# Kernel tuning notes

Measured on AMD Instinct MI355X. Metric: run time of the kernel, lower is better.

## Reference

```python
import jax, jax.numpy as jnp
import numpy as np

N = 2097152

def _net(x, W1, b1, W2, b2, W3, b3):
    # Net: 4 -> 64 -> 64 -> 1 MLP with ReLU
    h = jax.nn.relu(x @ W1 + b1)
    h = jax.nn.relu(h @ W2 + b2)
    return h @ W3 + b3  # [..., 1]

def setup_inputs() -> dict:
    key = jax.random.key(0)
    ks = jax.random.split(key, 7)
    def init_w(k, fan_in, fan_out):
        return (jax.random.normal(k, (fan_in, fan_out), jnp.float32)
                * np.float32(np.sqrt(2.0 / fan_in)))
    return {
        "states": jax.random.normal(ks[0], (N, 4), jnp.float32),
        "W1": init_w(ks[1], 4, 64),
        "b1": jnp.zeros((64,), jnp.float32),
        "W2": init_w(ks[2], 64, 64),
        "b2": jnp.zeros((64,), jnp.float32),
        "W3": init_w(ks[3], 64, 1),
        "b3": jnp.zeros((1,), jnp.float32),
    }

def reference(states, W1, b1, W2, b2, W3, b3):
    # log Q(s) = net(s) - log(sum_i exp(net(e_i))) ; loss = -sum_s log Q(s)
    logits = _net(states, W1, b1, W2, b2, W3, b3)            # [N, 1]
    denom_logits = _net(jnp.eye(4, dtype=states.dtype),       # 4 one-hot states
                        W1, b1, W2, b2, W3, b3)               # [4, 1]
    log_denom = jax.nn.logsumexp(denom_logits)                # scalar
    n = jnp.asarray(states.shape[0], states.dtype)
    loss = -(jnp.sum(logits) - n * log_denom)
    return loss.reshape(1)  # original accumulates shape-[1] tensors
```

## Files before the change

kernel.cpp:

```cpp
#include <hip/hip_runtime.h>
#include <hip/hip_bf16.h>
#include <hip/hip_fp16.h>
#include <stdint.h>

typedef __bf16 bf16x8 __attribute__((ext_vector_type(8)));
typedef float  f32x4  __attribute__((ext_vector_type(4)));
typedef _Float16 h2   __attribute__((ext_vector_type(2)));
typedef int    i32x4  __attribute__((ext_vector_type(4)));

#define MAIN_BLOCKS 1024

__global__ __launch_bounds__(256) void qloss_main(
    const float* __restrict__ states, const float* __restrict__ W1,
    const float* __restrict__ b1, const float* __restrict__ W2,
    const float* __restrict__ b2, const float* __restrict__ W3,
    int n_states, double* __restrict__ partials)
{
    const int lane = threadIdx.x & 63;
    const int wave = threadIdx.x >> 6;
    const int g = lane >> 4;
    const int r = lane & 15;

    float b1r[16];
    h2 w1p[2][16];
#pragma unroll
    for (int j = 0; j < 16; ++j) {
        const int k = 8*g + (j & 7) + 32*(j >> 3);
        b1r[j] = b1[k];
        w1p[0][j] = h2{(_Float16)W1[0*64 + k], (_Float16)W1[1*64 + k]};
        w1p[1][j] = h2{(_Float16)W1[2*64 + k], (_Float16)W1[3*64 + k]};
    }

    bf16x8 w2f[4][2];
#pragma unroll
    for (int t = 0; t < 4; ++t)
#pragma unroll
        for (int ks = 0; ks < 2; ++ks)
#pragma unroll
            for (int e = 0; e < 8; ++e) {
                const int k = 8*g + e + 32*ks;
                w2f[t][ks][e] = (__bf16)W2[k*64 + (r + 16*t)];
            }

    float b2r[4], w3r[4];
#pragma unroll
    for (int t = 0; t < 4; ++t) { b2r[t] = b2[r + 16*t]; w3r[t] = W3[r + 16*t]; }

#pragma unroll
    for (int j = 0; j < 16; ++j) {
        asm("" : "+v"(b1r[j]));
        asm("" : "+v"(w1p[0][j]), "+v"(w1p[1][j]));
    }
#pragma unroll
    for (int t = 0; t < 4; ++t) {
        asm("" : "+v"(w2f[t][0]), "+v"(w2f[t][1]));
        asm("" : "+v"(b2r[t]), "+v"(w3r[t]));
    }

    const int ntiles = n_states >> 4;
    const int waves_per_blk = blockDim.x >> 6;
    const int nwaves = gridDim.x * waves_per_blk;
    const float4* __restrict__ st4 = (const float4*)states;

    float ps0 = 0.f, ps1 = 0.f;
    const int tile0 = blockIdx.x * waves_per_blk + wave;
    float4 xc = {0.f, 0.f, 0.f, 0.f};
    if (tile0 < ntiles) xc = st4[tile0*16 + r];

    for (int tile = tile0; tile < ntiles; tile += nwaves) {
        const int nxt = tile + nwaves;
        const int nidx = (nxt < ntiles) ? nxt : tile;
        const float4 xn = st4[nidx*16 + r];

        const h2 x01 = {(_Float16)xc.x, (_Float16)xc.y};
        const h2 x23 = {(_Float16)xc.z, (_Float16)xc.w};
        i32x4 aw0, aw1;
#pragma unroll
        for (int ks = 0; ks < 2; ++ks) {
#pragma unroll
            for (int w = 0; w < 4; ++w) {
                const int j0 = ks*8 + 2*w, j1 = j0 + 1;
                float t0 = __builtin_amdgcn_fdot2(x01, w1p[0][j0], b1r[j0], false);
                t0       = __builtin_amdgcn_fdot2(x23, w1p[1][j0], t0, false);
                float t1 = __builtin_amdgcn_fdot2(x01, w1p[0][j1], b1r[j1], false);
                t1       = __builtin_amdgcn_fdot2(x23, w1p[1][j1], t1, false);
                t0 = fmaxf(t0, 0.f);
                t1 = fmaxf(t1, 0.f);
                int w32;
                asm("v_cvt_pk_bf16_f32 %0, %1, %2" : "=v"(w32) : "v"(t0), "v"(t1));
                if (ks == 0) aw0[w] = w32; else aw1[w] = w32;
            }
        }
        const bf16x8 af0 = __builtin_bit_cast(bf16x8, aw0);
        const bf16x8 af1 = __builtin_bit_cast(bf16x8, aw1);

#pragma unroll
        for (int t4 = 0; t4 < 4; ++t4) {
            f32x4 acc = { b2r[t4], b2r[t4], b2r[t4], b2r[t4] };
            acc = __builtin_amdgcn_mfma_f32_16x16x32_bf16(af0, w2f[t4][0], acc, 0, 0, 0);
            acc = __builtin_amdgcn_mfma_f32_16x16x32_bf16(af1, w2f[t4][1], acc, 0, 0, 0);
            ps0 = fmaf(fmaxf(acc[0], 0.f), w3r[t4], ps0);
            ps1 = fmaf(fmaxf(acc[1], 0.f), w3r[t4], ps1);
            ps0 = fmaf(fmaxf(acc[2], 0.f), w3r[t4], ps0);
            ps1 = fmaf(fmaxf(acc[3], 0.f), w3r[t4], ps1);
        }

        xc = xn;
    }

    float psum = ps0 + ps1;
#pragma unroll
    for (int off = 32; off; off >>= 1) psum += __shfl_xor(psum, off, 64);
    __shared__ float wpart[4];
    if (lane == 0) wpart[wave] = psum;
    __syncthreads();
    if (threadIdx.x == 0)
        partials[blockIdx.x] = (double)(wpart[0] + wpart[1] + wpart[2] + wpart[3]);
}

__global__ __launch_bounds__(256) void qloss_finalize(
    const float* __restrict__ W1, const float* __restrict__ b1,
    const float* __restrict__ W2, const float* __restrict__ b2,
    const float* __restrict__ W3, const float* __restrict__ b3,
    const double* __restrict__ partials, int nparts,
    int n_states, float* __restrict__ out)
{
    const int lane = threadIdx.x & 63;
    const int wave = threadIdx.x >> 6;

    __shared__ float  dlog[4];
    __shared__ double wsum[4];

    float h1 = fmaxf(W1[wave*64 + lane] + b1[lane], 0.f);
    float acc = b2[lane];
    for (int k = 0; k < 64; ++k)
        acc = fmaf(__shfl(h1, k, 64), W2[k*64 + lane], acc);
    float c = fmaxf(acc, 0.f) * W3[lane];
#pragma unroll
    for (int off = 32; off; off >>= 1) c += __shfl_xor(c, off, 64);
    if (lane == 0) dlog[wave] = c + b3[0];

    double ps = 0.0;
    for (int i = threadIdx.x; i < nparts; i += blockDim.x) ps += partials[i];
#pragma unroll
    for (int off = 32; off; off >>= 1) ps += __shfl_xor(ps, off, 64);
    if (lane == 0) wsum[wave] = ps;

    __syncthreads();
    if (threadIdx.x == 0) {
        const double S = wsum[0] + wsum[1] + wsum[2] + wsum[3];
        double m = dlog[0];
        for (int i = 1; i < 4; ++i) m = fmax(m, (double)dlog[i]);
        double e = 0.0;
        for (int i = 0; i < 4; ++i) e += exp((double)dlog[i] - m);
        const double lse = m + log(e);
        const double nn = (double)n_states;
        const double logits_sum = S + nn * (double)b3[0];
        out[0] = (float)(-(logits_sum - nn * lse));
    }
}

extern "C" void kernel_launch(void* const* d_in, const int* in_sizes, int n_in,
                              void* d_out, int out_size, void* d_ws, size_t ws_size,
                              hipStream_t stream)
{
    const float* states = (const float*)d_in[0];
    const float* W1 = (const float*)d_in[1];
    const float* b1 = (const float*)d_in[2];
    const float* W2 = (const float*)d_in[3];
    const float* b2 = (const float*)d_in[4];
    const float* W3 = (const float*)d_in[5];
    const float* b3 = (const float*)d_in[6];
    float* out = (float*)d_out;

    const int n_states = in_sizes[0] / 4;

    int nb = MAIN_BLOCKS;
    const size_t max_parts = ws_size / sizeof(double);
    if ((size_t)nb > max_parts) nb = (int)max_parts;
    if (nb < 1) nb = 1;
    double* partials = (double*)d_ws;

    qloss_main<<<nb, 256, 0, stream>>>(states, W1, b1, W2, b2, W3, n_states, partials);
    qloss_finalize<<<1, 256, 0, stream>>>(W1, b1, W2, b2, W3, b3, partials, nb, n_states, out);
}
```

Baseline: 52.93 us.

## Process two tiles per loop iteration and double grid size

Each wave now processes a pair of 16-row tiles per iteration, with independent accumulators, and prefetches both tiles of the next pair. This gives more independent MFMA and dot-product chains to hide latency and halves loop overhead. The grid is also doubled to 2048 blocks for more parallelism. A tail path handles an odd tile count. The cost is higher register pressure, which may reduce occupancy.

```diff
diff --git a/kernel.cpp b/kernel.cpp
--- a/kernel.cpp
+++ b/kernel.cpp
@@ -8,7 +8,7 @@
 typedef _Float16 h2   __attribute__((ext_vector_type(2)));
 typedef int    i32x4  __attribute__((ext_vector_type(4)));
 
-#define MAIN_BLOCKS 1024
+#define MAIN_BLOCKS 2048
 
 __global__ __launch_bounds__(256) void qloss_main(
     const float* __restrict__ states, const float* __restrict__ W1,
@@ -57,21 +57,9 @@
         asm("" : "+v"(b2r[t]), "+v"(w3r[t]));
     }
 
-    const int ntiles = n_states >> 4;
-    const int waves_per_blk = blockDim.x >> 6;
-    const int nwaves = gridDim.x * waves_per_blk;
-    const float4* __restrict__ st4 = (const float4*)states;
-
-    float ps0 = 0.f, ps1 = 0.f;
-    const int tile0 = blockIdx.x * waves_per_blk + wave;
-    float4 xc = {0.f, 0.f, 0.f, 0.f};
-    if (tile0 < ntiles) xc = st4[tile0*16 + r];
-
-    for (int tile = tile0; tile < ntiles; tile += nwaves) {
-        const int nxt = tile + nwaves;
-        const int nidx = (nxt < ntiles) ? nxt : tile;
-        const float4 xn = st4[nidx*16 + r];
-
+    float ps0 = 0.f, ps1 = 0.f, ps2 = 0.f, ps3 = 0.f;
+
+    auto do_tile = [&](const float4& xc, float& psA, float& psB) {
         const h2 x01 = {(_Float16)xc.x, (_Float16)xc.y};
         const h2 x23 = {(_Float16)xc.z, (_Float16)xc.w};
         i32x4 aw0, aw1;
@@ -93,22 +81,49 @@
         }
         const bf16x8 af0 = __builtin_bit_cast(bf16x8, aw0);
         const bf16x8 af1 = __builtin_bit_cast(bf16x8, aw1);
-
 #pragma unroll
         for (int t4 = 0; t4 < 4; ++t4) {
             f32x4 acc = { b2r[t4], b2r[t4], b2r[t4], b2r[t4] };
             acc = __builtin_amdgcn_mfma_f32_16x16x32_bf16(af0, w2f[t4][0], acc, 0, 0, 0);
             acc = __builtin_amdgcn_mfma_f32_16x16x32_bf16(af1, w2f[t4][1], acc, 0, 0, 0);
-            ps0 = fmaf(fmaxf(acc[0], 0.f), w3r[t4], ps0);
-            ps1 = fmaf(fmaxf(acc[1], 0.f), w3r[t4], ps1);
-            ps0 = fmaf(fmaxf(acc[2], 0.f), w3r[t4], ps0);
-            ps1 = fmaf(fmaxf(acc[3], 0.f), w3r[t4], ps1);
+            psA = fmaf(fmaxf(acc[0], 0.f), w3r[t4], psA);
+            psB = fmaf(fmaxf(acc[1], 0.f), w3r[t4], psB);
+            psA = fmaf(fmaxf(acc[2], 0.f), w3r[t4], psA);
+            psB = fmaf(fmaxf(acc[3], 0.f), w3r[t4], psB);
         }
-
-        xc = xn;
-    }
-
-    float psum = ps0 + ps1;
+    };
+
+    const int ntiles = n_states >> 4;
+    const int npairs = ntiles >> 1;
+    const int waves_per_blk = blockDim.x >> 6;
+    const int nwaves = gridDim.x * waves_per_blk;
+    const float4* __restrict__ st4 = (const float4*)states;
+
+    const int p0 = blockIdx.x * waves_per_blk + wave;
+    float4 xa = {0.f,0.f,0.f,0.f}, xb = {0.f,0.f,0.f,0.f};
+    if (p0 < npairs) {
+        xa = st4[p0*32 + r];
+        xb = st4[p0*32 + 16 + r];
+    }
+
+    for (int p = p0; p < npairs; p += nwaves) {
+        const int nxt = p + nwaves;
+        const int nidx = (nxt < npairs) ? nxt : p;
+        const float4 xan = st4[nidx*32 + r];
+        const float4 xbn = st4[nidx*32 + 16 + r];
+
+        do_tile(xa, ps0, ps1);
+        do_tile(xb, ps2, ps3);
+
+        xa = xan; xb = xbn;
+    }
+
+    if ((ntiles & 1) && blockIdx.x == 0 && wave == 0) {
+        const float4 xl = st4[(ntiles - 1)*16 + r];
+        do_tile(xl, ps0, ps1);
+    }
+
+    float psum = (ps0 + ps1) + (ps2 + ps3);
 #pragma unroll
     for (int off = 32; off; off >>= 1) psum += __shfl_xor(psum, off, 64);
     __shared__ float wpart[4];
```

Measured after the change: 57.87 us. 9.3% more time.
